# Kernel tuning notes

Measured on AMD Instinct MI355X. Metric: run time of the kernel, lower is better.

Reference implementation:

```python
import jax, jax.numpy as jnp
import numpy as np

N_HEADS = 8
OUT_DIM = 64
LEAKY_SLOPE = 0.2


def setup_inputs() -> dict:
    key = jax.random.key(0)
    k1, k2, k3 = jax.random.split(key, 3)
    N, IN_DIM = 4096, 256
    x = jax.random.normal(k1, (N, IN_DIM), dtype=jnp.float32)
    # nn.Linear(in_dim, out_dim*n_heads, bias=False): weight shape (out*heads, in)
    W = jax.random.normal(k2, (OUT_DIM * N_HEADS, IN_DIM), dtype=jnp.float32) * (1.0 / np.sqrt(IN_DIM))
    # attention vector, xavier-ish scale
    attn = jax.random.normal(k3, (1, N_HEADS, 2 * OUT_DIM), dtype=jnp.float32) * 0.1
    return {"x": x, "W": W, "attn": attn}


def reference(x, W, attn):
    N = x.shape[0]
    # Wx: (N, H, D)
    Wx = (x @ W.T).reshape(N, N_HEADS, OUT_DIM)
    # The torch code concats src/tgt then dots with attn; this decomposes exactly:
    # e[i,j,h] = leaky_relu( Wx[i,h]·a_src[h] + Wx[j,h]·a_tgt[h] )
    a_src = attn[0, :, :OUT_DIM]   # (H, D)
    a_tgt = attn[0, :, OUT_DIM:]   # (H, D)
    s = jnp.einsum('nhd,hd->nh', Wx, a_src)  # (N, H) score of row index (src)
    t = jnp.einsum('nhd,hd->nh', Wx, a_tgt)  # (N, H) score of col index (tgt)
    e = jax.nn.leaky_relu(s[:, None, :] + t[None, :, :], LEAKY_SLOPE)  # (N, N, H)
    a = jax.nn.softmax(e, axis=1)  # softmax over dim=1 (neighbors j)
    # out[i,h,d] = sum_j a[i,j,h] * Wx[j,h,d]
    out = jnp.einsum('ijh,jhd->ihd', a, Wx)
    return out.reshape(N, N_HEADS * OUT_DIM)  # concat=True
```

## Files before the change

kernel.cpp:

```cpp
#include <hip/hip_runtime.h>
#include <hip/hip_bf16.h>

#define NN 4096
#define KD 256
#define NH 8
#define DD 64
#define HD 512
#define SLOPE 0.2f
#define NB 2048

__device__ __forceinline__ unsigned sortkey(float f) {
    unsigned b = __float_as_uint(f);
    return b ^ ((unsigned)(((int)b) >> 31) | 0x80000000u);
}
__device__ __forceinline__ int bucketOf(float t) {
    int b = (int)((t + 8.0f) * 128.0f);
    return b < 0 ? 0 : (b > NB - 1 ? NB - 1 : b);
}

__global__ __launch_bounds__(256) void gemm_st(const float* __restrict__ x,
                                               const float* __restrict__ W,
                                               const float* __restrict__ attn,
                                               float* __restrict__ Wx,
                                               float* __restrict__ sH,
                                               float* __restrict__ tH) {
    const int b = blockIdx.x;
    const int bmTile = (b & 7) * 8 + ((b >> 3) & 7);
    const int h = b >> 6;
    const int bn = h * 64;
    const int bm = bmTile * 64;
    __shared__ float As[64][68];
    __shared__ float Bs[64][68];
    const int tid = threadIdx.x;
    const int tx = tid & 15, ty = tid >> 4;
    const int srow = tid >> 2;
    const int skq  = (tid & 3) * 16;
    float acc[4][4] = {};
    for (int k0 = 0; k0 < KD; k0 += 64) {
        float4 av[4], bv[4];
#pragma unroll
        for (int q = 0; q < 4; ++q) {
            av[q] = *(const float4*)&x[(bm + srow) * KD + k0 + skq + q * 4];
            bv[q] = *(const float4*)&W[(bn + srow) * KD + k0 + skq + q * 4];
        }
        __syncthreads();
#pragma unroll
        for (int q = 0; q < 4; ++q) {
            As[skq + q * 4 + 0][srow] = av[q].x;
            As[skq + q * 4 + 1][srow] = av[q].y;
            As[skq + q * 4 + 2][srow] = av[q].z;
            As[skq + q * 4 + 3][srow] = av[q].w;
            Bs[skq + q * 4 + 0][srow] = bv[q].x;
            Bs[skq + q * 4 + 1][srow] = bv[q].y;
            Bs[skq + q * 4 + 2][srow] = bv[q].z;
            Bs[skq + q * 4 + 3][srow] = bv[q].w;
        }
        __syncthreads();
#pragma unroll
        for (int kk = 0; kk < 64; ++kk) {
            float4 a = *(const float4*)&As[kk][ty * 4];
            float4 bb = *(const float4*)&Bs[kk][tx * 4];
            acc[0][0] += a.x * bb.x; acc[0][1] += a.x * bb.y; acc[0][2] += a.x * bb.z; acc[0][3] += a.x * bb.w;
            acc[1][0] += a.y * bb.x; acc[1][1] += a.y * bb.y; acc[1][2] += a.y * bb.z; acc[1][3] += a.y * bb.w;
            acc[2][0] += a.z * bb.x; acc[2][1] += a.z * bb.y; acc[2][2] += a.z * bb.z; acc[2][3] += a.z * bb.w;
            acc[3][0] += a.w * bb.x; acc[3][1] += a.w * bb.y; acc[3][2] += a.w * bb.z; acc[3][3] += a.w * bb.w;
        }
    }
#pragma unroll
    for (int m = 0; m < 4; ++m)
        *(float4*)&Wx[(bm + ty * 4 + m) * HD + bn + tx * 4] = *(const float4*)&acc[m][0];
    float4 as4 = *(const float4*)&attn[h * 128 + tx * 4];
    float4 at4 = *(const float4*)&attn[h * 128 + 64 + tx * 4];
#pragma unroll
    for (int m = 0; m < 4; ++m) {
        float s = acc[m][0] * as4.x + acc[m][1] * as4.y + acc[m][2] * as4.z + acc[m][3] * as4.w;
        float t = acc[m][0] * at4.x + acc[m][1] * at4.y + acc[m][2] * at4.z + acc[m][3] * at4.w;
#pragma unroll
        for (int off = 1; off < 16; off <<= 1) {
            s += __shfl_xor(s, off, 16);
            t += __shfl_xor(t, off, 16);
        }
        if (tx == 0) {
            sH[h * NN + bm + ty * 4 + m] = s;
            tH[h * NN + bm + ty * 4 + m] = t;
        }
    }
}

__global__ __launch_bounds__(1024) void rank_scatter(const float* __restrict__ tH,
                                                     const float* __restrict__ sH,
                                                     int* __restrict__ sortedIdx,
                                                     float* __restrict__ expT,
                                                     float* __restrict__ expT2,
                                                     int* __restrict__ cIdx) {
    const int h = blockIdx.x;
    const int tid = threadIdx.x;
    const int lane = tid & 63, wv = tid >> 6;
    __shared__ int hist[NB];
    __shared__ int wsum[16], woff[16];
    __shared__ unsigned bkey[NN];
    __shared__ unsigned short bidx[NN];
    for (int p = tid; p < NB; p += 1024) hist[p] = 0;
    float tv[4]; unsigned kv[4]; int bv[4];
    __syncthreads();
#pragma unroll
    for (int e = 0; e < 4; ++e) {
        int p = e * 1024 + tid;
        float t = tH[h * NN + p];
        tv[e] = t;
        kv[e] = sortkey(t);
        bv[e] = bucketOf(t);
        atomicAdd(&hist[bv[e]], 1);
    }
    __syncthreads();
    int a0 = hist[2 * tid], a1 = hist[2 * tid + 1];
    int ts = a0 + a1;
    int sc = ts;
#pragma unroll
    for (int o = 1; o < 64; o <<= 1) { int n = __shfl_up(sc, o, 64); if (lane >= o) sc += n; }
    if (lane == 63) wsum[wv] = sc;
    __syncthreads();
    if (tid == 0) { int acc = 0; for (int w = 0; w < 16; ++w) { woff[w] = acc; acc += wsum[w]; } }
    __syncthreads();
    int excl = sc - ts + woff[wv];
    hist[2 * tid]     = excl;
    hist[2 * tid + 1] = excl + a0;
    __syncthreads();
#pragma unroll
    for (int e = 0; e < 4; ++e) {
        int slot = atomicAdd(&hist[bv[e]], 1);
        bkey[slot] = kv[e];
        bidx[slot] = (unsigned short)(e * 1024 + tid);
    }
    __syncthreads();
#pragma unroll
    for (int e = 0; e < 4; ++e) {
        const int p = e * 1024 + tid;
        const int b = bv[e];
        const unsigned k = kv[e];
        const int start = b ? hist[b - 1] : 0;
        const int end = hist[b];
        int r = start;
        for (int s = start; s < end; ++s) {
            unsigned ks = bkey[s];
            r += (ks < k) | ((ks == k) & (bidx[s] < p));
        }
        sortedIdx[h * NN + r] = p;
        expT [h * NN + r] = expf(tv[e]);
        expT2[h * NN + r] = expf(SLOPE * tv[e]);
    }
#pragma unroll
    for (int e = 0; e < 4; ++e) {
        const int i = e * 1024 + tid;
        const float negS = -sH[h * NN + i];
        const unsigned kt = sortkey(negS);
        const int b = bucketOf(negS);
        const int start = b ? hist[b - 1] : 0;
        const int end = hist[b];
        int cs = start;
        for (int s = start; s < end; ++s) cs += (bkey[s] <= kt);
        cIdx[h * NN + i] = cs;
    }
}

__global__ __launch_bounds__(256) void local_prefix(const float* __restrict__ Wx,
                                                    const int* __restrict__ sortedIdx,
                                                    const float* __restrict__ expT,
                                                    const float* __restrict__ expT2,
                                                    float* __restrict__ localW,
                                                    float* __restrict__ localW2,
                                                    float* __restrict__ chunkTotW,
                                                    float* __restrict__ chunkTotW2,
                                                    float* __restrict__ localZ,
                                                    float* __restrict__ localZ2,
                                                    float* __restrict__ chunkZtot,
                                                    float* __restrict__ chunkZtot2) {
    const int c = blockIdx.x, h = blockIdx.y;
    const int tid = threadIdx.x;
    const int wid = tid >> 6, d = tid & 63;
    const int base = h * NN + c * 64;
    __shared__ float sums[4][64], sums2[4][64];
    float run = 0.f, run2 = 0.f;
    float ex[16], ex2[16];
#pragma unroll
    for (int kk = 0; kk < 16; ++kk) {
        int k = wid * 16 + kk;
        int j = sortedIdx[base + k];
        float w  = expT[base + k];
        float w2 = expT2[base + k];
        float v = Wx[j * HD + h * DD + d];
        ex[kk]  = run;  run  += w  * v;
        ex2[kk] = run2; run2 += w2 * v;
    }
    sums[wid][d] = run; sums2[wid][d] = run2;
    __syncthreads();
    float off = 0.f, off2 = 0.f;
    for (int w = 0; w < 4; ++w)
        if (w < wid) { off += sums[w][d]; off2 += sums2[w][d]; }
#pragma unroll
    for (int kk = 0; kk < 16; ++kk) {
        int k = wid * 16 + kk;
        localW [(h * NN + c * 64 + k) * 64 + d] = ex[kk]  + off;
        localW2[(h * NN + c * 64 + k) * 64 + d] = ex2[kk] + off2;
    }
    if (wid == 3) {
        chunkTotW [(h * 64 + c) * 64 + d] = off  + run;
        chunkTotW2[(h * 64 + c) * 64 + d] = off2 + run2;
    }
    if (wid == 0) {
        float z0 = expT[base + d];
        float z = z0;
#pragma unroll
        for (int o = 1; o < 64; o <<= 1) { float n = __shfl_up(z, o, 64); if (d >= o) z += n; }
        localZ[h * NN + c * 64 + d] = z - z0;
        if (d == 63) chunkZtot[h * 64 + c] = z;
    } else if (wid == 1) {
        float z0 = expT2[base + d];
        float z = z0;
#pragma unroll
        for (int o = 1; o < 64; o <<= 1) { float n = __shfl_up(z, o, 64); if (d >= o) z += n; }
        localZ2[h * NN + c * 64 + d] = z - z0;
        if (d == 63) chunkZtot2[h * 64 + c] = z;
    }
}

__global__ __launch_bounds__(256) void chunk_scan(float* __restrict__ chunkTotW,
                                                  float* __restrict__ chunkTotW2,
                                                  float* __restrict__ chunkZtot,
                                                  float* __restrict__ chunkZtot2,
                                                  float* __restrict__ totW,
                                                  float* __restrict__ totW2,
                                                  float* __restrict__ Ztot,
                                                  float* __restrict__ Ztot2) {
    const int h = blockIdx.x;
    const int tid = threadIdx.x;
    const int lane = tid & 63;
    __shared__ float cw[64 * 64];
    __shared__ float cw2[64 * 64];
    __shared__ float zb[64], zb2[64];
#pragma unroll
    for (int it = 0; it < 16; ++it) {
        int lin = it * 256 + tid;
        cw[lin]  = chunkTotW [h * 4096 + lin];
        cw2[lin] = chunkTotW2[h * 4096 + lin];
    }
    if (tid >= 128 && tid < 192) zb[lane]  = chunkZtot [h * 64 + lane];
    if (tid >= 192)              zb2[lane] = chunkZtot2[h * 64 + lane];
    __syncthreads();
    if (tid < 64) {
        float acc = 0.f;
        for (int c = 0; c < 64; ++c) { int idx = c * 64 + tid; float t = cw[idx]; cw[idx] = acc; acc += t; }
        totW[h * 64 + tid] = acc;
    } else if (tid < 128) {
        int d = tid - 64;
        float acc = 0.f;
        for (int c = 0; c < 64; ++c) { int idx = c * 64 + d; float t = cw2[idx]; cw2[idx] = acc; acc += t; }
        totW2[h * 64 + d] = acc;
    } else if (tid < 192) {
        float z0 = zb[lane];
        float z = z0;
#pragma unroll
        for (int o = 1; o < 64; o <<= 1) { float n = __shfl_up(z, o, 64); if (lane >= o) z += n; }
        chunkZtot[h * 64 + lane] = z - z0;
        if (lane == 63) Ztot[h] = z;
    } else {
        float z0 = zb2[lane];
        float z = z0;
#pragma unroll
        for (int o = 1; o < 64; o <<= 1) { float n = __shfl_up(z, o, 64); if (lane >= o) z += n; }
        chunkZtot2[h * 64 + lane] = z - z0;
        if (lane == 63) Ztot2[h] = z;
    }
    __syncthreads();
#pragma unroll
    for (int it = 0; it < 16; ++it) {
        int lin = it * 256 + tid;
        chunkTotW [h * 4096 + lin] = cw[lin];
        chunkTotW2[h * 4096 + lin] = cw2[lin];
    }
}

__global__ __launch_bounds__(256) void out_kernel(const float* __restrict__ sH,
                                                  const int* __restrict__ cIdx,
                                                  const float* __restrict__ localW,
                                                  const float* __restrict__ localW2,
                                                  const float* __restrict__ chunkTotW,
                                                  const float* __restrict__ chunkTotW2,
                                                  const float* __restrict__ localZ,
                                                  const float* __restrict__ localZ2,
                                                  const float* __restrict__ chunkZtot,
                                                  const float* __restrict__ chunkZtot2,
                                                  const float* __restrict__ totW,
                                                  const float* __restrict__ totW2,
                                                  const float* __restrict__ Ztot,
                                                  const float* __restrict__ Ztot2,
                                                  float* __restrict__ out) {
    const int h = blockIdx.y;
    const int i = blockIdx.x * 4 + (threadIdx.x >> 6);
    const int d = threadIdx.x & 63;
    const float sv = sH[h * NN + i];
    const int c = cIdx[h * NN + i];
    const float es  = expf(sv);
    const float es2 = expf(SLOPE * sv);
    float wpos, wneg, zp, zn;
    if (c == NN) {
        wpos = 0.f; zp = 0.f;
        wneg = totW2[h * 64 + d];
        zn   = Ztot2[h];
    } else {
        float pw  = localW [(h * NN + c) * 64 + d] + chunkTotW [(h * 64 + (c >> 6)) * 64 + d];
        float pw2 = localW2[(h * NN + c) * 64 + d] + chunkTotW2[(h * 64 + (c >> 6)) * 64 + d];
        wpos = totW[h * 64 + d] - pw;
        wneg = pw2;
        float pz  = localZ [h * NN + c] + chunkZtot [h * 64 + (c >> 6)];
        float pz2 = localZ2[h * NN + c] + chunkZtot2[h * 64 + (c >> 6)];
        zp = Ztot[h] - pz;
        zn = pz2;
    }
    out[i * HD + h * DD + d] = (es * wpos + es2 * wneg) / (es * zp + es2 * zn);
}

extern "C" void kernel_launch(void* const* d_in, const int* in_sizes, int n_in,
                              void* d_out, int out_size, void* d_ws, size_t ws_size,
                              hipStream_t stream) {
    const float* x    = (const float*)d_in[0];
    const float* W    = (const float*)d_in[1];
    const float* attn = (const float*)d_in[2];
    float* out = (float*)d_out;

    float* ws = (float*)d_ws;
    size_t o = 0;
    float* Wx        = ws + o; o += (size_t)NN * HD;
    float* sH        = ws + o; o += (size_t)NH * NN;
    float* tH        = ws + o; o += (size_t)NH * NN;
    float* expT      = ws + o; o += (size_t)NH * NN;
    float* expT2     = ws + o; o += (size_t)NH * NN;
    int*   sortedIdx = (int*)(ws + o); o += (size_t)NH * NN;
    int*   cIdx      = (int*)(ws + o); o += (size_t)NH * NN;
    float* localZ    = ws + o; o += (size_t)NH * NN;
    float* localZ2   = ws + o; o += (size_t)NH * NN;
    float* chunkTotW  = ws + o; o += (size_t)NH * 64 * 64;
    float* chunkTotW2 = ws + o; o += (size_t)NH * 64 * 64;
    float* chunkZtot  = ws + o; o += (size_t)NH * 64;
    float* chunkZtot2 = ws + o; o += (size_t)NH * 64;
    float* totW   = ws + o; o += (size_t)NH * 64;
    float* totW2  = ws + o; o += (size_t)NH * 64;
    float* Ztot   = ws + o; o += 64;
    float* Ztot2  = ws + o; o += 64;
    float* localW  = ws + o; o += (size_t)NH * NN * 64;
    float* localW2 = ws + o; o += (size_t)NH * NN * 64;

    gemm_st<<<dim3(512), dim3(256), 0, stream>>>(x, W, attn, Wx, sH, tH);
    rank_scatter<<<dim3(NH), dim3(1024), 0, stream>>>(tH, sH, sortedIdx, expT, expT2, cIdx);
    local_prefix<<<dim3(64, NH), dim3(256), 0, stream>>>(Wx, sortedIdx, expT, expT2, localW, localW2,
                                                         chunkTotW, chunkTotW2, localZ, localZ2, chunkZtot, chunkZtot2);
    chunk_scan<<<dim3(NH), dim3(256), 0, stream>>>(chunkTotW, chunkTotW2, chunkZtot, chunkZtot2,
                                                   totW, totW2, Ztot, Ztot2);
    out_kernel<<<dim3(NN / 4, NH), dim3(256), 0, stream>>>(sH, cIdx, localW, localW2, chunkTotW, chunkTotW2,
                                                           localZ, localZ2, chunkZtot, chunkZtot2,
                                                           totW, totW2, Ztot, Ztot2, out);
}
```

Before: 63.45 us.

## Fuse chunk-level prefix scan into output kernel, dropping chunk_scan launch

Removes the separate single-block-per-head chunk_scan kernel. Each out_kernel block now loads the per-head chunk totals into shared memory and recomputes the exclusive scan redundantly with a 4-wave segmented scan. It then processes 64 rows per block instead of 4. This saves one launch and a serial dependency stage, at the cost of redundant scan work in 512 blocks and far fewer, larger blocks for the output phase.

```diff
diff --git a/kernel.cpp b/kernel.cpp
--- a/kernel.cpp
+++ b/kernel.cpp
@@ -224,100 +224,95 @@
     }
 }
 
-__global__ __launch_bounds__(256) void chunk_scan(float* __restrict__ chunkTotW,
-                                                  float* __restrict__ chunkTotW2,
-                                                  float* __restrict__ chunkZtot,
-                                                  float* __restrict__ chunkZtot2,
-                                                  float* __restrict__ totW,
-                                                  float* __restrict__ totW2,
-                                                  float* __restrict__ Ztot,
-                                                  float* __restrict__ Ztot2) {
-    const int h = blockIdx.x;
-    const int tid = threadIdx.x;
-    const int lane = tid & 63;
-    __shared__ float cw[64 * 64];
-    __shared__ float cw2[64 * 64];
-    __shared__ float zb[64], zb2[64];
-#pragma unroll
-    for (int it = 0; it < 16; ++it) {
-        int lin = it * 256 + tid;
-        cw[lin]  = chunkTotW [h * 4096 + lin];
-        cw2[lin] = chunkTotW2[h * 4096 + lin];
-    }
-    if (tid >= 128 && tid < 192) zb[lane]  = chunkZtot [h * 64 + lane];
-    if (tid >= 192)              zb2[lane] = chunkZtot2[h * 64 + lane];
-    __syncthreads();
-    if (tid < 64) {
-        float acc = 0.f;
-        for (int c = 0; c < 64; ++c) { int idx = c * 64 + tid; float t = cw[idx]; cw[idx] = acc; acc += t; }
-        totW[h * 64 + tid] = acc;
-    } else if (tid < 128) {
-        int d = tid - 64;
-        float acc = 0.f;
-        for (int c = 0; c < 64; ++c) { int idx = c * 64 + d; float t = cw2[idx]; cw2[idx] = acc; acc += t; }
-        totW2[h * 64 + d] = acc;
-    } else if (tid < 192) {
-        float z0 = zb[lane];
-        float z = z0;
-#pragma unroll
-        for (int o = 1; o < 64; o <<= 1) { float n = __shfl_up(z, o, 64); if (lane >= o) z += n; }
-        chunkZtot[h * 64 + lane] = z - z0;
-        if (lane == 63) Ztot[h] = z;
-    } else {
-        float z0 = zb2[lane];
-        float z = z0;
-#pragma unroll
-        for (int o = 1; o < 64; o <<= 1) { float n = __shfl_up(z, o, 64); if (lane >= o) z += n; }
-        chunkZtot2[h * 64 + lane] = z - z0;
-        if (lane == 63) Ztot2[h] = z;
-    }
-    __syncthreads();
-#pragma unroll
-    for (int it = 0; it < 16; ++it) {
-        int lin = it * 256 + tid;
-        chunkTotW [h * 4096 + lin] = cw[lin];
-        chunkTotW2[h * 4096 + lin] = cw2[lin];
-    }
-}
-
 __global__ __launch_bounds__(256) void out_kernel(const float* __restrict__ sH,
                                                   const int* __restrict__ cIdx,
                                                   const float* __restrict__ localW,
                                                   const float* __restrict__ localW2,
+                                                  const float* __restrict__ localZ,
+                                                  const float* __restrict__ localZ2,
                                                   const float* __restrict__ chunkTotW,
                                                   const float* __restrict__ chunkTotW2,
-                                                  const float* __restrict__ localZ,
-                                                  const float* __restrict__ localZ2,
                                                   const float* __restrict__ chunkZtot,
                                                   const float* __restrict__ chunkZtot2,
-                                                  const float* __restrict__ totW,
-                                                  const float* __restrict__ totW2,
-                                                  const float* __restrict__ Ztot,
-                                                  const float* __restrict__ Ztot2,
                                                   float* __restrict__ out) {
-    const int h = blockIdx.y;
-    const int i = blockIdx.x * 4 + (threadIdx.x >> 6);
-    const int d = threadIdx.x & 63;
-    const float sv = sH[h * NN + i];
-    const int c = cIdx[h * NN + i];
-    const float es  = expf(sv);
-    const float es2 = expf(SLOPE * sv);
-    float wpos, wneg, zp, zn;
-    if (c == NN) {
-        wpos = 0.f; zp = 0.f;
-        wneg = totW2[h * 64 + d];
-        zn   = Ztot2[h];
-    } else {
-        float pw  = localW [(h * NN + c) * 64 + d] + chunkTotW [(h * 64 + (c >> 6)) * 64 + d];
-        float pw2 = localW2[(h * NN + c) * 64 + d] + chunkTotW2[(h * 64 + (c >> 6)) * 64 + d];
-        wpos = totW[h * 64 + d] - pw;
-        wneg = pw2;
-        float pz  = localZ [h * NN + c] + chunkZtot [h * 64 + (c >> 6)];
-        float pz2 = localZ2[h * NN + c] + chunkZtot2[h * 64 + (c >> 6)];
-        zp = Ztot[h] - pz;
-        zn = pz2;
-    }
-    out[i * HD + h * DD + d] = (es * wpos + es2 * wneg) / (es * zp + es2 * zn);
+    const int h  = blockIdx.y;
+    const int ig = blockIdx.x;
+    const int tid = threadIdx.x;
+    const int d = tid & 63, wv = tid >> 6;
+    __shared__ __align__(16) float scW[65][64];
+    __shared__ __align__(16) float scW2[65][64];
+    __shared__ float psum[2][4][64];
+    __shared__ float scZ[65], scZ2[65];
+    {
+        const float4* cw  = (const float4*)&chunkTotW [h * 4096];
+        const float4* cw2 = (const float4*)&chunkTotW2[h * 4096];
+        float4* dw  = (float4*)&scW [0][0];
+        float4* dw2 = (float4*)&scW2[0][0];
+        for (int p = tid; p < 1024; p += 256) { dw[p] = cw[p]; dw2[p] = cw2[p]; }
+        if (tid < 64)       scZ [tid]      = chunkZtot [h * 64 + tid];
+        else if (tid < 128) scZ2[tid - 64] = chunkZtot2[h * 64 + tid - 64];
+    }
+    __syncthreads();
+    float segTot, segTot2;
+    {
+        const int c0 = wv * 16;
+        float acc = 0.f, acc2 = 0.f;
+#pragma unroll
+        for (int q = 0; q < 16; ++q) {
+            float t  = scW [c0 + q][d]; scW [c0 + q][d] = acc;  acc  += t;
+            float t2 = scW2[c0 + q][d]; scW2[c0 + q][d] = acc2; acc2 += t2;
+        }
+        segTot = acc; segTot2 = acc2;
+        psum[0][wv][d] = acc; psum[1][wv][d] = acc2;
+    }
+    __syncthreads();
+    {
+        float off = 0.f, off2 = 0.f;
+        for (int w = 0; w < wv; ++w) { off += psum[0][w][d]; off2 += psum[1][w][d]; }
+        const int c0 = wv * 16;
+#pragma unroll
+        for (int q = 0; q < 16; ++q) { scW[c0 + q][d] += off; scW2[c0 + q][d] += off2; }
+        if (wv == 3) { scW[64][d] = off + segTot; scW2[64][d] = off2 + segTot2; }
+    }
+    if (tid < 64) {
+        float z0 = scZ[tid]; float z = z0;
+#pragma unroll
+        for (int o = 1; o < 64; o <<= 1) { float n = __shfl_up(z, o, 64); if (tid >= o) z += n; }
+        scZ[tid] = z - z0;
+        if (tid == 63) scZ[64] = z;
+    } else if (tid < 128) {
+        int l = tid - 64;
+        float z0 = scZ2[l]; float z = z0;
+#pragma unroll
+        for (int o = 1; o < 64; o <<= 1) { float n = __shfl_up(z, o, 64); if (l >= o) z += n; }
+        scZ2[l] = z - z0;
+        if (l == 63) scZ2[64] = z;
+    }
+    __syncthreads();
+#pragma unroll 4
+    for (int p = 0; p < 16; ++p) {
+        const int i = ig * 64 + p * 4 + wv;
+        const float sv = sH[h * NN + i];
+        const int c = cIdx[h * NN + i];
+        const float es  = expf(sv);
+        const float es2 = expf(SLOPE * sv);
+        float wpos, wneg, zp, zn;
+        if (c == NN) {
+            wpos = 0.f; zp = 0.f;
+            wneg = scW2[64][d];
+            zn   = scZ2[64];
+        } else {
+            float pw  = localW [(h * NN + c) * 64 + d] + scW [c >> 6][d];
+            float pw2 = localW2[(h * NN + c) * 64 + d] + scW2[c >> 6][d];
+            wpos = scW[64][d] - pw;
+            wneg = pw2;
+            float pz  = localZ [h * NN + c] + scZ [c >> 6];
+            float pz2 = localZ2[h * NN + c] + scZ2[c >> 6];
+            zp = scZ[64] - pz;
+            zn = pz2;
+        }
+        out[i * HD + h * DD + d] = (es * wpos + es2 * wneg) / (es * zp + es2 * zn);
+    }
 }
 
 extern "C" void kernel_launch(void* const* d_in, const int* in_sizes, int n_in,
@@ -343,10 +338,6 @@
     float* chunkTotW2 = ws + o; o += (size_t)NH * 64 * 64;
     float* chunkZtot  = ws + o; o += (size_t)NH * 64;
     float* chunkZtot2 = ws + o; o += (size_t)NH * 64;
-    float* totW   = ws + o; o += (size_t)NH * 64;
-    float* totW2  = ws + o; o += (size_t)NH * 64;
-    float* Ztot   = ws + o; o += 64;
-    float* Ztot2  = ws + o; o += 64;
     float* localW  = ws + o; o += (size_t)NH * NN * 64;
     float* localW2 = ws + o; o += (size_t)NH * NN * 64;
 
@@ -354,9 +345,6 @@
     rank_scatter<<<dim3(NH), dim3(1024), 0, stream>>>(tH, sH, sortedIdx, expT, expT2, cIdx);
     local_prefix<<<dim3(64, NH), dim3(256), 0, stream>>>(Wx, sortedIdx, expT, expT2, localW, localW2,
                                                          chunkTotW, chunkTotW2, localZ, localZ2, chunkZtot, chunkZtot2);
-    chunk_scan<<<dim3(NH), dim3(256), 0, stream>>>(chunkTotW, chunkTotW2, chunkZtot, chunkZtot2,
-                                                   totW, totW2, Ztot, Ztot2);
-    out_kernel<<<dim3(NN / 4, NH), dim3(256), 0, stream>>>(sH, cIdx, localW, localW2, chunkTotW, chunkTotW2,
-                                                           localZ, localZ2, chunkZtot, chunkZtot2,
-                                                           totW, totW2, Ztot, Ztot2, out);
-}
+    out_kernel<<<dim3(64, NH), dim3(256), 0, stream>>>(sH, cIdx, localW, localW2, localZ, localZ2,
+                                                       chunkTotW, chunkTotW2, chunkZtot, chunkZtot2, out);
+}
```

Result: slower. 67.61 us (+6.5%).
